# Kernel optimization log

Measured on AMD Instinct MI355X. Metric: run time of the kernel, lower is better.

Reference implementation:

```python
import jax, jax.numpy as jnp
import numpy as np

B, T, C, H = 4, 4096, 1024, 128

def setup_inputs() -> dict:
    key = jax.random.key(0)
    k1, k2, k3, k4 = jax.random.split(key, 4)
    s = 1.0 / np.sqrt(C)  # roughly match nn.Linear init scale
    return {
        "xd": jax.random.normal(k1, (B, T, C), dtype=jnp.float32),
        "Wq": jax.random.normal(k2, (C, H), dtype=jnp.float32) * s,
        "Wk": jax.random.normal(k3, (C, H), dtype=jnp.float32) * s,
        "Wv": jax.random.normal(k4, (C, H), dtype=jnp.float32) * s,
    }

def reference(xd, Wq, Wk, Wv):
    # self-attention path (xe is None): k, q, v all from xd
    q = jnp.einsum("btc,ch->bth", xd, Wq)
    k = jnp.einsum("btc,ch->bth", xd, Wk)
    v = jnp.einsum("btc,ch->bth", xd, Wv)
    scale = jnp.asarray(k.shape[-1], q.dtype) ** -0.5
    wei = jnp.einsum("bqh,bkh->bqk", q, k) * scale  # [B, T, T]
    # causal mask (masking=True): tril == 0 -> -inf
    causal = jnp.tril(jnp.ones((xd.shape[1], xd.shape[1]), dtype=bool))
    wei = jnp.where(causal[None, :, :], wei, jnp.asarray(-jnp.inf, wei.dtype))
    wei = jax.nn.softmax(wei, axis=-1)
    # dropout: eval-mode identity (deterministic reference)
    out = jnp.einsum("bqk,bkh->bqh", wei, v)  # [B, T, H]
    return out
```

## Files before the change

### kernel.cpp

```cpp
#include <hip/hip_runtime.h>
#include <math.h>

typedef __bf16 bf16x8 __attribute__((ext_vector_type(8)));
typedef float f32x4 __attribute__((ext_vector_type(4)));
typedef float f32x16 __attribute__((ext_vector_type(16)));
typedef unsigned int u32x4 __attribute__((ext_vector_type(4)));
typedef unsigned short u16x8 __attribute__((ext_vector_type(8)));

#define B_ 4
#define T_ 4096
#define C_ 1024
#define H_ 128

static __device__ __forceinline__ unsigned short f32_to_bf16(float f) {
  unsigned int u = __builtin_bit_cast(unsigned int, f);
  u += 0x7FFFu + ((u >> 16) & 1u);
  return (unsigned short)(u >> 16);
}
static __device__ __forceinline__ float bf16_to_f32(unsigned short u) {
  unsigned int x = ((unsigned int)u) << 16;
  return __builtin_bit_cast(float, x);
}

static __device__ __forceinline__ bf16x8 ld16g(const unsigned short* p) {
  return __builtin_bit_cast(bf16x8, *(const u32x4*)p);
}

static __device__ __forceinline__ f32x4 mfma16(bf16x8 a, bf16x8 b, f32x4 c) {
  return __builtin_amdgcn_mfma_f32_16x16x32_bf16(a, b, c, 0, 0, 0);
}
static __device__ __forceinline__ f32x16 mfma32(bf16x8 a, bf16x8 b, f32x16 c) {
  return __builtin_amdgcn_mfma_f32_32x32x16_bf16(a, b, c, 0, 0, 0);
}

static __device__ __forceinline__ void swapu(unsigned int& a, unsigned int& b) {
  asm volatile("v_permlane32_swap_b32 %0, %1" : "+v"(a), "+v"(b));
}
static __device__ __forceinline__ unsigned int cvtpk(float lo, float hi) {
  unsigned int r;
  asm("v_cvt_pk_bf16_f32 %0, %1, %2" : "=v"(r) : "v"(lo), "v"(hi));
  return r;
}
static __device__ __forceinline__ float bpermf(int addr, float v) {
  return __builtin_bit_cast(float, __builtin_amdgcn_ds_bpermute(addr, __builtin_bit_cast(int, v)));
}
static __device__ __forceinline__ float half_merge_max(float x) {
  return fmaxf(x, __shfl_xor(x, 32));
}
static __device__ __forceinline__ float half_merge_sum(float x) {
  return x + __shfl_xor(x, 32);
}
static __device__ __forceinline__ float vmax16(f32x16 v) {
  float a0 = fmaxf(v[0], v[1]),  a1 = fmaxf(v[2], v[3]);
  float a2 = fmaxf(v[4], v[5]),  a3 = fmaxf(v[6], v[7]);
  float a4 = fmaxf(v[8], v[9]),  a5 = fmaxf(v[10], v[11]);
  float a6 = fmaxf(v[12], v[13]), a7 = fmaxf(v[14], v[15]);
  float b0 = fmaxf(a0, a1), b1 = fmaxf(a2, a3), b2 = fmaxf(a4, a5), b3 = fmaxf(a6, a7);
  return fmaxf(fmaxf(b0, b1), fmaxf(b2, b3));
}
static __device__ __forceinline__ float vsum16(f32x16 v) {
  float a0 = v[0] + v[1],  a1 = v[2] + v[3],  a2 = v[4] + v[5],  a3 = v[6] + v[7];
  float a4 = v[8] + v[9],  a5 = v[10] + v[11], a6 = v[12] + v[13], a7 = v[14] + v[15];
  float b0 = a0 + a1, b1 = a2 + a3, b2 = a4 + a5, b3 = a6 + a7;
  return (b0 + b1) + (b2 + b3);
}

typedef __attribute__((address_space(1))) const unsigned char as1_u8;
typedef __attribute__((address_space(3))) unsigned char as3_u8;
static __device__ __forceinline__ void async16(const void* g, void* l) {
  __builtin_amdgcn_global_load_lds((as1_u8*)g, (as3_u8*)l, 16, 0, 0);
}

static __device__ __forceinline__ u16x8 pack8(float4 a, float4 b) {
  u16x8 w;
  w[0] = f32_to_bf16(a.x); w[1] = f32_to_bf16(a.y);
  w[2] = f32_to_bf16(a.z); w[3] = f32_to_bf16(a.w);
  w[4] = f32_to_bf16(b.x); w[5] = f32_to_bf16(b.y);
  w[6] = f32_to_bf16(b.z); w[7] = f32_to_bf16(b.w);
  return w;
}

#define PART_BYTES 33792

__global__ __launch_bounds__(256) void conv_w_kernel(const float* __restrict__ W0,
                                                     const float* __restrict__ W1,
                                                     const float* __restrict__ W2,
                                                     unsigned short* __restrict__ WT,
                                                     float qscale) {
  int tid = blockIdx.x * 256 + threadIdx.x;
  int o = tid >> 17;
  int r = tid & 131071;
  int n = r & 127;
  int k = r >> 7;
  const float* W = (o == 0) ? W0 : ((o == 1) ? W1 : W2);
  float v = W[r];
  if (o == 0) v *= qscale;
  WT[(size_t)o * 131072 + (size_t)n * 1024 + k] = f32_to_bf16(v);
}

__global__ __launch_bounds__(256) void qkv_fused_kernel(const float* __restrict__ X,
                                                        const unsigned short* __restrict__ WT,
                                                        unsigned short* __restrict__ Qb,
                                                        unsigned short* __restrict__ K3,
                                                        unsigned short* __restrict__ V3) {
  __shared__ __align__(16) unsigned short At[128 * 64];
  __shared__ __align__(16) unsigned short Bt[128 * 64];
  const int bid = blockIdx.x;
  const int xcd = bid & 7, ii = bid >> 3;
  const int o = ii % 3;
  const int tile = (ii / 3) * 8 + xcd;

  const float* Ax = X + (size_t)tile * 128 * 1024;
  const unsigned short* Bsrc = WT + (size_t)o * 131072;

  const int tid = threadIdx.x;
  const int lane = tid & 63, wid = tid >> 6;
  const int l15 = lane & 15, lg = lane >> 4;
  const int srow = wid * 8 + (lane >> 3);
  const int scol = (lane & 7) * 8;
  const int swcol = scol ^ ((srow & 7) << 3);
  const int sbcol = (((lane & 7) ^ (lane >> 3)) << 3);
  const int wm = wid >> 1, wn = wid & 1;
  const int rsw = (l15 & 7) << 3;

  const f32x4 fzero = {0.f, 0.f, 0.f, 0.f};
  f32x4 acc[4][4];
#pragma unroll
  for (int i = 0; i < 4; i++)
#pragma unroll
    for (int j = 0; j < 4; j++) acc[i][j] = fzero;

  float4 fA[4][2];
#pragma unroll
  for (int i4 = 0; i4 < 4; i4++) {
    const float* xs = Ax + (size_t)(i4 * 32 + srow) * 1024 + scol;
    fA[i4][0] = *(const float4*)xs;
    fA[i4][1] = *(const float4*)(xs + 4);
  }

  for (int ks = 0; ks < 16; ks++) {
    const int k0 = ks * 64;
    __syncthreads();
#pragma unroll
    for (int i4 = 0; i4 < 4; i4++)
      async16(Bsrc + (size_t)(i4 * 32 + srow) * 1024 + k0 + sbcol, &Bt[(i4 * 32 + wid * 8) * 64]);
#pragma unroll
    for (int i4 = 0; i4 < 4; i4++) {
      const int row = i4 * 32 + srow;
      *(u16x8*)(&At[row * 64 + swcol]) = pack8(fA[i4][0], fA[i4][1]);
    }
    __syncthreads();
    if (ks + 1 < 16) {
#pragma unroll
      for (int i4 = 0; i4 < 4; i4++) {
        const float* xs = Ax + (size_t)(i4 * 32 + srow) * 1024 + (ks + 1) * 64 + scol;
        fA[i4][0] = *(const float4*)xs;
        fA[i4][1] = *(const float4*)(xs + 4);
      }
    }
#pragma unroll
    for (int kk = 0; kk < 2; kk++) {
      bf16x8 af[4], bfr[4];
#pragma unroll
      for (int i = 0; i < 4; i++)
        af[i] = ld16g(&At[(wm * 64 + i * 16 + l15) * 64 + ((kk * 32 + lg * 8) ^ rsw)]);
#pragma unroll
      for (int j = 0; j < 4; j++)
        bfr[j] = ld16g(&Bt[(wn * 64 + j * 16 + l15) * 64 + ((kk * 32 + lg * 8) ^ rsw)]);
      __builtin_amdgcn_s_setprio(1);
#pragma unroll
      for (int i = 0; i < 4; i++)
#pragma unroll
        for (int j = 0; j < 4; j++) acc[i][j] = mfma16(af[i], bfr[j], acc[i][j]);
      __builtin_amdgcn_s_setprio(0);
    }
  }

  if (o == 0) {
#pragma unroll
    for (int i = 0; i < 4; i++)
#pragma unroll
      for (int j = 0; j < 4; j++)
#pragma unroll
        for (int r = 0; r < 4; r++) {
          int row = tile * 128 + wm * 64 + i * 16 + lg * 4 + r;
          int col = wn * 64 + j * 16 + l15;
          Qb[(size_t)row * 128 + col] = f32_to_bf16(acc[i][j][r]);
        }
  } else if (o == 1) {
#pragma unroll
    for (int i = 0; i < 4; i++)
#pragma unroll
      for (int j = 0; j < 4; j++)
#pragma unroll
        for (int r = 0; r < 4; r++) {
          int token = tile * 128 + wm * 64 + i * 16 + lg * 4 + r;
          int d = wn * 64 + j * 16 + l15;
          int bb = token >> 12, t = token & 4095;
          int t32 = t >> 5;
          int lane2 = (t & 31) | (((d >> 3) & 1) << 5);
          int c = d >> 4;
          int j2 = d & 7;
          K3[(size_t)(((bb * 128 + t32) * 8 + c) * 64 + lane2) * 8 + j2] = f32_to_bf16(acc[i][j][r]);
        }
  } else {
#pragma unroll
    for (int i = 0; i < 4; i++)
#pragma unroll
      for (int j = 0; j < 4; j++)
#pragma unroll
        for (int r = 0; r < 4; r++) {
          int token = tile * 128 + wm * 64 + i * 16 + lg * 4 + r;
          int d = wn * 64 + j * 16 + l15;
          int bb = token >> 12, tt = token & 4095;
          int t32 = tt >> 5;
          int kss = (tt >> 4) & 1;
          int hi2 = (tt >> 3) & 1;
          int j2 = tt & 7;
          int dt = d >> 5;
          int lane2 = (d & 31) | (hi2 << 5);
          V3[(size_t)(((bb * 128 + t32) * 8 + dt * 2 + kss) * 64 + lane2) * 8 + j2] = f32_to_bf16(acc[i][j][r]);
        }
  }
}

__global__ __launch_bounds__(256, 2) void attn_kernel(const unsigned short* __restrict__ Qb,
                                                      const unsigned short* __restrict__ K3,
                                                      const unsigned short* __restrict__ V3,
                                                      unsigned char* __restrict__ Pw8) {
  const int bid = blockIdx.x;
  const int xcd = bid & 7;
  const int b = xcd >> 1;
  const int rest = bid >> 3;
  const int h = rest % 6;
  const int jj = rest / 6;
  const int g = (xcd & 1) + 2 * (15 - jj);

  const int tid = threadIdx.x;
  const int wid = tid >> 6, lane = tid & 63;
  const int l31 = lane & 31, hi = lane >> 5;
  const int qbase = g * 128 + wid * 32;

  __shared__ __align__(16) unsigned char LDSraw[32768];
  unsigned short* lbuf = (unsigned short*)LDSraw;

  const unsigned short* K3b = K3 + (size_t)b * 524288;
  const unsigned short* V3b = V3 + (size_t)b * 524288;
  const int jmax_w = 4 * g + wid;
  const int Jcap = 4 * g + 3;
  const int R = (Jcap >= h) ? ((Jcap - h) / 6 + 1) : 0;

  const unsigned short* qp = Qb + ((size_t)(b * T_ + qbase + l31) << 7) + hi * 8;
  bf16x8 qf[8];
#pragma unroll
  for (int c = 0; c < 8; c++) qf[c] = ld16g(qp + c * 16);

  const f32x16 z16 = {0.f,0.f,0.f,0.f,0.f,0.f,0.f,0.f,0.f,0.f,0.f,0.f,0.f,0.f,0.f,0.f};
  f32x16 o[4];
  o[0] = z16; o[1] = z16; o[2] = z16; o[3] = z16;
  float m = -1e30f, l = 0.f;
  const int addrbase = hi << 4;

  const unsigned short* sbase = (wid < 2) ? K3b : V3b;
  const int soff = (wid & 1) * 2048;
  const int region = ((wid >= 2) ? 4096 : 0) + soff;

  if (R > 0) {
    const unsigned short* s0 = sbase + (size_t)h * 4096 + soff + lane * 8;
    unsigned short* d0 = lbuf + region;
#pragma unroll
    for (int i = 0; i < 4; i++) async16(s0 + i * 512, d0 + i * 512);
  }

  for (int r = 0; r < R; r++) {
    const int cur = r & 1;
    if (r + 1 < R) {
      const int jS = h + 6 * (r + 1);
      const unsigned short* sN = sbase + (size_t)jS * 4096 + soff + lane * 8;
      unsigned short* dN = lbuf + (cur ^ 1) * 8192 + region;
#pragma unroll
      for (int i = 0; i < 4; i++) async16(sN + i * 512, dN + i * 512);
      asm volatile("s_waitcnt vmcnt(4)" ::: "memory");
    } else {
      asm volatile("s_waitcnt vmcnt(0)" ::: "memory");
    }
    __builtin_amdgcn_s_barrier();

    const int j = h + 6 * r;
    if (j <= jmax_w) {
      const unsigned short* Kl = lbuf + cur * 8192;
      const unsigned short* Vl = Kl + 4096;
      bf16x8 kf[8];
#pragma unroll
      for (int c = 0; c < 8; c++) kf[c] = ld16g(Kl + c * 512 + lane * 8);
      f32x16 s = z16;
      __builtin_amdgcn_s_setprio(1);
#pragma unroll
      for (int c = 0; c < 8; c++) s = mfma32(kf[c], qf[c], s);
      __builtin_amdgcn_s_setprio(0);

      bf16x8 vf[4][2];
#pragma unroll
      for (int dt = 0; dt < 4; dt++)
#pragma unroll
        for (int ks = 0; ks < 2; ks++)
          vf[dt][ks] = ld16g(Vl + (dt * 2 + ks) * 512 + lane * 8);

      if (j == jmax_w) {
        const int kvb = j << 5;
        const int qq = qbase + l31;
#pragma unroll
        for (int r2 = 0; r2 < 16; r2++) {
          const int c0 = (r2 & 3) + 8 * (r2 >> 2) + 4 * hi;
          if (kvb + c0 > qq) s[r2] = -1e30f;
        }
      }

      float pm = half_merge_max(vmax16(s));
      const bool skip = __all(pm - m <= 8.0f);
      float mn = skip ? m : fmaxf(m, pm);
#pragma unroll
      for (int r2 = 0; r2 < 16; r2++) s[r2] = exp2f(s[r2] - mn);
      float ps = half_merge_sum(vsum16(s));
      if (skip) {
        l = l + ps;
      } else {
        float al = exp2f(m - mn);
        m = mn;
        l = l * al + ps;
#pragma unroll
        for (int r2 = 0; r2 < 16; r2++) {
          const int addr = addrbase + 4 * ((r2 & 3) + 8 * (r2 >> 2));
          float alb = bpermf(addr, al);
          o[0][r2] *= alb; o[1][r2] *= alb; o[2][r2] *= alb; o[3][r2] *= alb;
        }
      }

      bf16x8 pa[2];
#pragma unroll
      for (int ks = 0; ks < 2; ks++) {
        const int gb = ks * 8;
        unsigned int xa = cvtpk(s[gb + 0], s[gb + 1]), xb = cvtpk(s[gb + 4], s[gb + 5]);
        swapu(xa, xb);
        unsigned int ya = cvtpk(s[gb + 2], s[gb + 3]), yb = cvtpk(s[gb + 6], s[gb + 7]);
        swapu(ya, yb);
        u32x4 pw; pw[0] = xa; pw[1] = ya; pw[2] = xb; pw[3] = yb;
        pa[ks] = __builtin_bit_cast(bf16x8, pw);
      }

      __builtin_amdgcn_s_setprio(1);
#pragma unroll
      for (int ks = 0; ks < 2; ks++)
#pragma unroll
        for (int dt = 0; dt < 4; dt++) o[dt] = mfma32(pa[ks], vf[dt][ks], o[dt]);
      __builtin_amdgcn_s_setprio(0);
    }
    __builtin_amdgcn_sched_barrier(0);
    __builtin_amdgcn_s_barrier();
  }

  unsigned char* Pb = Pw8 + (size_t)((b * 32 + g) * 6 + h) * PART_BYTES;
  unsigned short* Po = (unsigned short*)Pb;
  float* Pm = (float*)(Pb + 32768);
  float* Pl = (float*)(Pb + 33280);
#pragma unroll
  for (int r2 = 0; r2 < 16; r2++) {
    const int q128 = wid * 32 + (r2 & 3) + 8 * (r2 >> 2) + 4 * hi;
#pragma unroll
    for (int dt = 0; dt < 4; dt++)
      Po[q128 * 128 + dt * 32 + l31] = f32_to_bf16(o[dt][r2]);
  }
  if (lane < 32) { Pm[wid * 32 + l31] = m; Pl[wid * 32 + l31] = l; }
}

__global__ __launch_bounds__(256) void attn_merge_kernel(const unsigned char* __restrict__ Pw8,
                                                         float* __restrict__ Out) {
  const int gid = blockIdx.x * 256 + threadIdx.x;
  const int tl = gid >> 12;
  const int inner = gid & 4095;
  const int q = inner >> 5;
  const int d = (inner & 31) * 4;
  const unsigned char* base = Pw8 + (size_t)tl * 6 * PART_BYTES;

  float mm[6], ll[6];
#pragma unroll
  for (int p = 0; p < 6; p++) {
    mm[p] = *(const float*)(base + p * PART_BYTES + 32768 + q * 4);
    ll[p] = *(const float*)(base + p * PART_BYTES + 33280 + q * 4);
  }
  float mn = mm[0];
#pragma unroll
  for (int p = 1; p < 6; p++) mn = fmaxf(mn, mm[p]);
  float f[6], denom = 0.f;
#pragma unroll
  for (int p = 0; p < 6; p++) { f[p] = exp2f(mm[p] - mn); denom += f[p] * ll[p]; }
  const float inv = 1.0f / denom;

  f32x4 acc = {0.f, 0.f, 0.f, 0.f};
#pragma unroll
  for (int p = 0; p < 6; p++) {
    const unsigned short* po = (const unsigned short*)(base + p * PART_BYTES) + q * 128 + d;
    unsigned long long v4 = *(const unsigned long long*)po;
    const unsigned short* pv = (const unsigned short*)&v4;
#pragma unroll
    for (int i = 0; i < 4; i++) acc[i] += f[p] * bf16_to_f32(pv[i]);
  }
#pragma unroll
  for (int i = 0; i < 4; i++) acc[i] *= inv;
  const int b = tl >> 5, g = tl & 31;
  *(f32x4*)(Out + (size_t)(b * 4096 + g * 128 + q) * 128 + d) = acc;
}

extern "C" void kernel_launch(void* const* d_in, const int* in_sizes, int n_in,
                              void* d_out, int out_size, void* d_ws, size_t ws_size,
                              hipStream_t stream) {
  const float* X  = (const float*)d_in[0];
  const float* W0 = (const float*)d_in[1];
  const float* W1 = (const float*)d_in[2];
  const float* W2 = (const float*)d_in[3];
  float* Out = (float*)d_out;

  unsigned char* ws = (unsigned char*)d_ws;
  unsigned short* WT = (unsigned short*)(ws);
  unsigned char* Pw  = ws;
  unsigned short* Qb = (unsigned short*)(ws + 34078720);
  unsigned short* K3 = (unsigned short*)(ws + 38273024);
  unsigned short* V3 = (unsigned short*)(ws + 42467328);

  const float qscale = 1.4426950408889634f / sqrtf(128.0f);

  conv_w_kernel<<<dim3(1536), dim3(256), 0, stream>>>(W0, W1, W2, WT, qscale);
  qkv_fused_kernel<<<dim3(384), dim3(256), 0, stream>>>(X, WT, Qb, K3, V3);
  attn_kernel<<<dim3(768), dim3(256), 0, stream>>>(Qb, K3, V3, Pw);
  attn_merge_kernel<<<dim3(2048), dim3(256), 0, stream>>>(Pw, Out);
}
```

Baseline: 73.04 us.

## Restructure QKV projection: 64-row tiles, double-buffered weights, direct A fragments

The QKV projection kernel now uses 64-token tiles instead of 128, so the grid doubles to 768 blocks and occupancy is hinted at 3 blocks per SM. The weight tile is double-buffered in LDS and prefetched one k-step ahead using async loads with explicit vmcnt waits. The X tile no longer goes through LDS: each lane loads its own MFMA A-fragment from global memory and converts it with packed bf16 conversion. This removes one barrier per step and the LDS round trip for A. In exchange, the weight matrix is reloaded twice as often, and the fp32 X reads use a less coalesced per-lane pattern.

```diff
diff --git a/kernel.cpp b/kernel.cpp
--- a/kernel.cpp
+++ b/kernel.cpp
@@ -71,13 +71,11 @@
   __builtin_amdgcn_global_load_lds((as1_u8*)g, (as3_u8*)l, 16, 0, 0);
 }
 
-static __device__ __forceinline__ u16x8 pack8(float4 a, float4 b) {
-  u16x8 w;
-  w[0] = f32_to_bf16(a.x); w[1] = f32_to_bf16(a.y);
-  w[2] = f32_to_bf16(a.z); w[3] = f32_to_bf16(a.w);
-  w[4] = f32_to_bf16(b.x); w[5] = f32_to_bf16(b.y);
-  w[6] = f32_to_bf16(b.z); w[7] = f32_to_bf16(b.w);
-  return w;
+static __device__ __forceinline__ bf16x8 cvt8(float4 a, float4 b) {
+  u32x4 w;
+  w[0] = cvtpk(a.x, a.y); w[1] = cvtpk(a.z, a.w);
+  w[2] = cvtpk(b.x, b.y); w[3] = cvtpk(b.z, b.w);
+  return __builtin_bit_cast(bf16x8, w);
 }
 
 #define PART_BYTES 33792
@@ -98,103 +96,126 @@
   WT[(size_t)o * 131072 + (size_t)n * 1024 + k] = f32_to_bf16(v);
 }
 
-__global__ __launch_bounds__(256) void qkv_fused_kernel(const float* __restrict__ X,
-                                                        const unsigned short* __restrict__ WT,
-                                                        unsigned short* __restrict__ Qb,
-                                                        unsigned short* __restrict__ K3,
-                                                        unsigned short* __restrict__ V3) {
-  __shared__ __align__(16) unsigned short At[128 * 64];
-  __shared__ __align__(16) unsigned short Bt[128 * 64];
+__global__ __launch_bounds__(256, 3) void qkv_fused_kernel(const float* __restrict__ X,
+                                                           const unsigned short* __restrict__ WT,
+                                                           unsigned short* __restrict__ Qb,
+                                                           unsigned short* __restrict__ K3,
+                                                           unsigned short* __restrict__ V3) {
+  __shared__ __align__(16) unsigned short Bt[2][128 * 64];
   const int bid = blockIdx.x;
   const int xcd = bid & 7, ii = bid >> 3;
   const int o = ii % 3;
   const int tile = (ii / 3) * 8 + xcd;
 
-  const float* Ax = X + (size_t)tile * 128 * 1024;
+  const float* Ax = X + (size_t)tile * 64 * 1024;
   const unsigned short* Bsrc = WT + (size_t)o * 131072;
 
   const int tid = threadIdx.x;
   const int lane = tid & 63, wid = tid >> 6;
   const int l15 = lane & 15, lg = lane >> 4;
-  const int srow = wid * 8 + (lane >> 3);
-  const int scol = (lane & 7) * 8;
-  const int swcol = scol ^ ((srow & 7) << 3);
-  const int sbcol = (((lane & 7) ^ (lane >> 3)) << 3);
   const int wm = wid >> 1, wn = wid & 1;
   const int rsw = (l15 & 7) << 3;
 
+  const int srow = wid * 8 + (lane >> 3);
+  const int sbcol = (((lane & 7) ^ (lane >> 3)) << 3);
+
+  const float* arow0 = Ax + (size_t)(wm * 32 + l15) * 1024 + lg * 8;
+  const float* arow1 = arow0 + 16 * 1024;
+
   const f32x4 fzero = {0.f, 0.f, 0.f, 0.f};
-  f32x4 acc[4][4];
-#pragma unroll
-  for (int i = 0; i < 4; i++)
+  f32x4 acc[2][4];
+#pragma unroll
+  for (int i = 0; i < 2; i++)
 #pragma unroll
     for (int j = 0; j < 4; j++) acc[i][j] = fzero;
 
-  float4 fA[4][2];
-#pragma unroll
-  for (int i4 = 0; i4 < 4; i4++) {
-    const float* xs = Ax + (size_t)(i4 * 32 + srow) * 1024 + scol;
-    fA[i4][0] = *(const float4*)xs;
-    fA[i4][1] = *(const float4*)(xs + 4);
+  float4 fA[2][2][2];
+
+#pragma unroll
+  for (int i4 = 0; i4 < 4; i4++)
+    async16(Bsrc + (size_t)(i4 * 32 + srow) * 1024 + sbcol,
+            &Bt[0][(i4 * 32 + wid * 8) * 64]);
+#pragma unroll
+  for (int i = 0; i < 2; i++) {
+    const float* ar = i ? arow1 : arow0;
+#pragma unroll
+    for (int kk = 0; kk < 2; kk++)
+#pragma unroll
+      for (int u = 0; u < 2; u++)
+        fA[i][kk][u] = *(const float4*)(ar + kk * 32 + u * 4);
   }
 
   for (int ks = 0; ks < 16; ks++) {
-    const int k0 = ks * 64;
-    __syncthreads();
-#pragma unroll
-    for (int i4 = 0; i4 < 4; i4++)
-      async16(Bsrc + (size_t)(i4 * 32 + srow) * 1024 + k0 + sbcol, &Bt[(i4 * 32 + wid * 8) * 64]);
-#pragma unroll
-    for (int i4 = 0; i4 < 4; i4++) {
-      const int row = i4 * 32 + srow;
-      *(u16x8*)(&At[row * 64 + swcol]) = pack8(fA[i4][0], fA[i4][1]);
+    const int cur = ks & 1;
+    if (ks < 15) {
+      const int k1 = (ks + 1) * 64;
+#pragma unroll
+      for (int i4 = 0; i4 < 4; i4++)
+        async16(Bsrc + (size_t)(i4 * 32 + srow) * 1024 + k1 + sbcol,
+                &Bt[cur ^ 1][(i4 * 32 + wid * 8) * 64]);
+      asm volatile("s_waitcnt vmcnt(4)" ::: "memory");
+    } else {
+      asm volatile("s_waitcnt vmcnt(0)" ::: "memory");
     }
-    __syncthreads();
-    if (ks + 1 < 16) {
-#pragma unroll
-      for (int i4 = 0; i4 < 4; i4++) {
-        const float* xs = Ax + (size_t)(i4 * 32 + srow) * 1024 + (ks + 1) * 64 + scol;
-        fA[i4][0] = *(const float4*)xs;
-        fA[i4][1] = *(const float4*)(xs + 4);
+
+    bf16x8 af[2][2];
+#pragma unroll
+    for (int i = 0; i < 2; i++)
+#pragma unroll
+      for (int kk = 0; kk < 2; kk++)
+        af[i][kk] = cvt8(fA[i][kk][0], fA[i][kk][1]);
+
+    if (ks < 15) {
+      const int k1 = (ks + 1) * 64;
+#pragma unroll
+      for (int i = 0; i < 2; i++) {
+        const float* ar = (i ? arow1 : arow0) + k1;
+#pragma unroll
+        for (int kk = 0; kk < 2; kk++)
+#pragma unroll
+          for (int u = 0; u < 2; u++)
+            fA[i][kk][u] = *(const float4*)(ar + kk * 32 + u * 4);
       }
     }
+
+    __builtin_amdgcn_s_barrier();
+
 #pragma unroll
     for (int kk = 0; kk < 2; kk++) {
-      bf16x8 af[4], bfr[4];
-#pragma unroll
-      for (int i = 0; i < 4; i++)
-        af[i] = ld16g(&At[(wm * 64 + i * 16 + l15) * 64 + ((kk * 32 + lg * 8) ^ rsw)]);
+      bf16x8 bfr[4];
 #pragma unroll
       for (int j = 0; j < 4; j++)
-        bfr[j] = ld16g(&Bt[(wn * 64 + j * 16 + l15) * 64 + ((kk * 32 + lg * 8) ^ rsw)]);
+        bfr[j] = ld16g(&Bt[cur][(wn * 64 + j * 16 + l15) * 64 + ((kk * 32 + lg * 8) ^ rsw)]);
       __builtin_amdgcn_s_setprio(1);
 #pragma unroll
-      for (int i = 0; i < 4; i++)
-#pragma unroll
-        for (int j = 0; j < 4; j++) acc[i][j] = mfma16(af[i], bfr[j], acc[i][j]);
+      for (int i = 0; i < 2; i++)
+#pragma unroll
+        for (int j = 0; j < 4; j++) acc[i][j] = mfma16(af[i][kk], bfr[j], acc[i][j]);
       __builtin_amdgcn_s_setprio(0);
     }
+    __builtin_amdgcn_sched_barrier(0);
+    __builtin_amdgcn_s_barrier();
   }
 
   if (o == 0) {
 #pragma unroll
-    for (int i = 0; i < 4; i++)
+    for (int i = 0; i < 2; i++)
 #pragma unroll
       for (int j = 0; j < 4; j++)
 #pragma unroll
         for (int r = 0; r < 4; r++) {
-          int row = tile * 128 + wm * 64 + i * 16 + lg * 4 + r;
+          int row = tile * 64 + wm * 32 + i * 16 + lg * 4 + r;
           int col = wn * 64 + j * 16 + l15;
           Qb[(size_t)row * 128 + col] = f32_to_bf16(acc[i][j][r]);
         }
   } else if (o == 1) {
 #pragma unroll
-    for (int i = 0; i < 4; i++)
+    for (int i = 0; i < 2; i++)
 #pragma unroll
       for (int j = 0; j < 4; j++)
 #pragma unroll
         for (int r = 0; r < 4; r++) {
-          int token = tile * 128 + wm * 64 + i * 16 + lg * 4 + r;
+          int token = tile * 64 + wm * 32 + i * 16 + lg * 4 + r;
           int d = wn * 64 + j * 16 + l15;
           int bb = token >> 12, t = token & 4095;
           int t32 = t >> 5;
@@ -205,12 +226,12 @@
         }
   } else {
 #pragma unroll
-    for (int i = 0; i < 4; i++)
+    for (int i = 0; i < 2; i++)
 #pragma unroll
       for (int j = 0; j < 4; j++)
 #pragma unroll
         for (int r = 0; r < 4; r++) {
-          int token = tile * 128 + wm * 64 + i * 16 + lg * 4 + r;
+          int token = tile * 64 + wm * 32 + i * 16 + lg * 4 + r;
           int d = wn * 64 + j * 16 + l15;
           int bb = token >> 12, tt = token & 4095;
           int t32 = tt >> 5;
@@ -430,7 +451,7 @@
   const float qscale = 1.4426950408889634f / sqrtf(128.0f);
 
   conv_w_kernel<<<dim3(1536), dim3(256), 0, stream>>>(W0, W1, W2, WT, qscale);
-  qkv_fused_kernel<<<dim3(384), dim3(256), 0, stream>>>(X, WT, Qb, K3, V3);
+  qkv_fused_kernel<<<dim3(768), dim3(256), 0, stream>>>(X, WT, Qb, K3, V3);
   attn_kernel<<<dim3(768), dim3(256), 0, stream>>>(Qb, K3, V3, Pw);
   attn_merge_kernel<<<dim3(2048), dim3(256), 0, stream>>>(Pw, Out);
 }
```

Measured after the change: 97.59 us. 33.6% more time.

## Double-buffer weight tile and prefetch X two steps ahead in QKV GEMM

Applied to the files above, without the earlier changes.

Restructures the QKV projection main loop into a software pipeline. The B (weight) tile is now double-buffered in LDS and loaded asynchronously one step ahead. X fp32 rows are held in two register sets and loaded two steps ahead. Explicit vmcnt waits plus raw s_barrier replace the two __syncthreads per step. This is meant to hide global-load latency behind MFMA work, at the cost of more registers and LDS, and it relies on a hand-counted vmcnt(12) being correct.

```diff
diff --git a/kernel.cpp b/kernel.cpp
--- a/kernel.cpp
+++ b/kernel.cpp
@@ -98,13 +98,63 @@
   WT[(size_t)o * 131072 + (size_t)n * 1024 + k] = f32_to_bf16(v);
 }
 
+#define QKV_STEP(KS, ACUR, CURBUF)                                                        \
+  {                                                                                       \
+    const int ks_ = (KS);                                                                 \
+    if (ks_ + 1 < 16) {                                                                   \
+      const int k1 = (ks_ + 1) * 64;                                                      \
+      _Pragma("unroll")                                                                   \
+      for (int i4 = 0; i4 < 4; i4++)                                                      \
+        async16(Bsrc + (size_t)(i4 * 32 + srow) * 1024 + k1 + sbcol,                      \
+                &Bt[CURBUF ^ 1][(i4 * 32 + wid * 8) * 64]);                               \
+    }                                                                                     \
+    _Pragma("unroll")                                                                     \
+    for (int i4 = 0; i4 < 4; i4++) {                                                      \
+      const int row_ = i4 * 32 + srow;                                                    \
+      *(u16x8*)(&At[row_ * 64 + swcol]) = pack8(ACUR[i4][0], ACUR[i4][1]);                \
+    }                                                                                     \
+    if (ks_ + 2 < 16) {                                                                   \
+      const int k2 = (ks_ + 2) * 64;                                                      \
+      _Pragma("unroll")                                                                   \
+      for (int i4 = 0; i4 < 4; i4++) {                                                    \
+        const float* xs = Ax + (size_t)(i4 * 32 + srow) * 1024 + k2 + scol;               \
+        ACUR[i4][0] = *(const float4*)xs;                                                 \
+        ACUR[i4][1] = *(const float4*)(xs + 4);                                           \
+      }                                                                                   \
+    }                                                                                     \
+    if (ks_ + 1 < 16) {                                                                   \
+      asm volatile("s_waitcnt vmcnt(12) lgkmcnt(0)" ::: "memory");                        \
+    } else {                                                                              \
+      asm volatile("s_waitcnt vmcnt(0) lgkmcnt(0)" ::: "memory");                         \
+    }                                                                                     \
+    __builtin_amdgcn_s_barrier();                                                         \
+    _Pragma("unroll")                                                                     \
+    for (int kk = 0; kk < 2; kk++) {                                                      \
+      bf16x8 af[4], bfr[4];                                                               \
+      _Pragma("unroll")                                                                   \
+      for (int i = 0; i < 4; i++)                                                         \
+        af[i] = ld16g(&At[(wm * 64 + i * 16 + l15) * 64 + ((kk * 32 + lg * 8) ^ rsw)]);   \
+      _Pragma("unroll")                                                                   \
+      for (int j = 0; j < 4; j++)                                                         \
+        bfr[j] = ld16g(&Bt[CURBUF][(wn * 64 + j * 16 + l15) * 64 + ((kk * 32 + lg * 8) ^ rsw)]); \
+      __builtin_amdgcn_s_setprio(1);                                                      \
+      _Pragma("unroll")                                                                   \
+      for (int i = 0; i < 4; i++)                                                         \
+        _Pragma("unroll")                                                                 \
+        for (int j = 0; j < 4; j++) acc[i][j] = mfma16(af[i], bfr[j], acc[i][j]);         \
+      __builtin_amdgcn_s_setprio(0);                                                      \
+    }                                                                                     \
+    __builtin_amdgcn_sched_barrier(0);                                                    \
+    __builtin_amdgcn_s_barrier();                                                         \
+  }
+
 __global__ __launch_bounds__(256) void qkv_fused_kernel(const float* __restrict__ X,
                                                         const unsigned short* __restrict__ WT,
                                                         unsigned short* __restrict__ Qb,
                                                         unsigned short* __restrict__ K3,
                                                         unsigned short* __restrict__ V3) {
   __shared__ __align__(16) unsigned short At[128 * 64];
-  __shared__ __align__(16) unsigned short Bt[128 * 64];
+  __shared__ __align__(16) unsigned short Bt[2][128 * 64];
   const int bid = blockIdx.x;
   const int xcd = bid & 7, ii = bid >> 3;
   const int o = ii % 3;
@@ -130,50 +180,29 @@
 #pragma unroll
     for (int j = 0; j < 4; j++) acc[i][j] = fzero;
 
-  float4 fA[4][2];
+  float4 fA_a[4][2];
+  float4 fA_b[4][2];
+
 #pragma unroll
   for (int i4 = 0; i4 < 4; i4++) {
     const float* xs = Ax + (size_t)(i4 * 32 + srow) * 1024 + scol;
-    fA[i4][0] = *(const float4*)xs;
-    fA[i4][1] = *(const float4*)(xs + 4);
-  }
-
-  for (int ks = 0; ks < 16; ks++) {
-    const int k0 = ks * 64;
-    __syncthreads();
-#pragma unroll
-    for (int i4 = 0; i4 < 4; i4++)
-      async16(Bsrc + (size_t)(i4 * 32 + srow) * 1024 + k0 + sbcol, &Bt[(i4 * 32 + wid * 8) * 64]);
-#pragma unroll
-    for (int i4 = 0; i4 < 4; i4++) {
-      const int row = i4 * 32 + srow;
-      *(u16x8*)(&At[row * 64 + swcol]) = pack8(fA[i4][0], fA[i4][1]);
-    }
-    __syncthreads();
-    if (ks + 1 < 16) {
-#pragma unroll
-      for (int i4 = 0; i4 < 4; i4++) {
-        const float* xs = Ax + (size_t)(i4 * 32 + srow) * 1024 + (ks + 1) * 64 + scol;
-        fA[i4][0] = *(const float4*)xs;
-        fA[i4][1] = *(const float4*)(xs + 4);
-      }
-    }
-#pragma unroll
-    for (int kk = 0; kk < 2; kk++) {
-      bf16x8 af[4], bfr[4];
-#pragma unroll
-      for (int i = 0; i < 4; i++)
-        af[i] = ld16g(&At[(wm * 64 + i * 16 + l15) * 64 + ((kk * 32 + lg * 8) ^ rsw)]);
-#pragma unroll
-      for (int j = 0; j < 4; j++)
-        bfr[j] = ld16g(&Bt[(wn * 64 + j * 16 + l15) * 64 + ((kk * 32 + lg * 8) ^ rsw)]);
-      __builtin_amdgcn_s_setprio(1);
-#pragma unroll
-      for (int i = 0; i < 4; i++)
-#pragma unroll
-        for (int j = 0; j < 4; j++) acc[i][j] = mfma16(af[i], bfr[j], acc[i][j]);
-      __builtin_amdgcn_s_setprio(0);
-    }
+    fA_a[i4][0] = *(const float4*)xs;
+    fA_a[i4][1] = *(const float4*)(xs + 4);
+  }
+#pragma unroll
+  for (int i4 = 0; i4 < 4; i4++) {
+    const float* xs = Ax + (size_t)(i4 * 32 + srow) * 1024 + 64 + scol;
+    fA_b[i4][0] = *(const float4*)xs;
+    fA_b[i4][1] = *(const float4*)(xs + 4);
+  }
+#pragma unroll
+  for (int i4 = 0; i4 < 4; i4++)
+    async16(Bsrc + (size_t)(i4 * 32 + srow) * 1024 + sbcol,
+            &Bt[0][(i4 * 32 + wid * 8) * 64]);
+
+  for (int ks = 0; ks < 16; ks += 2) {
+    QKV_STEP(ks,     fA_a, 0)
+    QKV_STEP(ks + 1, fA_b, 1)
   }
 
   if (o == 0) {
```

New measurement: 75.73 us. 3.7% more time.
